# Kernel optimization log

Measured on AMD Instinct MI355X. Metric: run time of the kernel, lower is better.

## Reference

```python
import jax, jax.numpy as jnp
import numpy as np

B, S, D = 8, 2048, 128

def setup_inputs() -> dict:
    key = jax.random.key(0)
    kq, kk, kv, km = jax.random.split(key, 4)
    q = jax.random.normal(kq, (B, S, D), dtype=jnp.float32)
    k = jax.random.normal(kk, (B, S, D), dtype=jnp.float32)
    v = jax.random.normal(kv, (B, S, D), dtype=jnp.float32)
    mask = jax.random.randint(km, (B, S), 0, 2).astype(bool)  # True = masked out
    return {"q": q, "k": k, "v": v, "mask": mask}

def reference(q, k, v, mask):
    scaler = np.sqrt(D).astype(np.float32)
    # score[b, i, j] = <q_i, k_j> / sqrt(d_k)
    score = jnp.einsum('bik,bjk->bij', q, k) / scaler
    score = score - jnp.max(score, axis=-1, keepdims=True)
    e = jnp.exp(score)
    # mask is (B, S_kv): broadcast across query positions, zero out masked keys
    e = jnp.where(mask[:, None, :], 0.0, e)
    a = e / jnp.sum(e, axis=-1, keepdims=True)
    c = jnp.einsum('bij,bjd->bid', a, v)
    return c
```

## Files before the change

kernel.cpp:

```cpp
#include <hip/hip_runtime.h>
#include <hip/hip_fp16.h>
#include <math.h>

typedef __attribute__((ext_vector_type(8))) short short8;
typedef __attribute__((ext_vector_type(4))) float floatx4;

namespace {
constexpr int Bn = 8;
constexpr int Sn = 2048;
constexpr int Dn = 128;
constexpr int BQ = 64;
constexpr int BK = 64;
constexpr int QTILES = Sn / BQ;
constexpr int NKB = Sn / BK;
constexpr int ROWS = Bn * Sn;
constexpr int NSPLIT = 4;
constexpr float SC2 = 0.12753102063642597f;
constexpr int TILE_USH = BK * Dn;
}

#if __has_builtin(__builtin_amdgcn_exp2f)
#define EXP2(x) __builtin_amdgcn_exp2f(x)
#else
#define EXP2(x) exp2f(x)
#endif

__device__ __forceinline__ unsigned short f2bf(float x) {
  union { float f; unsigned u; } a; a.f = x;
  unsigned r = a.u + 0x7fffu + ((a.u >> 16) & 1u);
  return (unsigned short)(r >> 16);
}

__device__ __forceinline__ void gl_lds16(const void* g, void* l, int lane) {
#if __has_builtin(__builtin_amdgcn_global_load_lds)
  (void)lane;
  __builtin_amdgcn_global_load_lds((const __attribute__((address_space(1))) unsigned int*)g,
                                   (__attribute__((address_space(3))) unsigned int*)l, 16, 0, 0);
#else
  *(float4*)((char*)l + lane * 16) = *(const float4*)g;
#endif
}

__global__ __launch_bounds__(256)
void prep(const float* __restrict__ kg, const float* __restrict__ vg,
          const unsigned char* __restrict__ mraw,
          unsigned short* __restrict__ Kpg, unsigned short* __restrict__ Vpg,
          float* __restrict__ mb2g) {
  __shared__ __align__(16) float Vf[16 * 136];
  const int p = blockIdx.x;
  const int b = p >> 7, q = p & 127;
  const int kb = q >> 2, k16 = q & 3;
  const int t = threadIdx.x;

  unsigned wv = ((const unsigned int*)mraw)[t];
  int any1  = __syncthreads_or((wv & 0x0000ff00u) ? 1 : 0);
  int any23 = __syncthreads_or((wv & 0xffff0000u) ? 1 : 0);
  const int mlayout = any1 ? 1 : (any23 ? 2 : 0);
  if (p < 64) {
    int idx = p * 256 + t;
    bool ms;
    if (mlayout == 1)      ms = mraw[idx] != 0;
    else if (mlayout == 2) ms = ((const float*)mraw)[idx] != 0.0f;
    else                   ms = ((const int*)mraw)[idx] != 0;
    mb2g[idx] = ms ? -1e30f : 0.0f;
  }

  const int j  = t >> 4;
  const int o8 = t & 15;
  const size_t base = ((size_t)(b * Sn + kb * 64 + k16 * 16 + j)) * 32 + o8 * 2;
  const float4* k4 = (const float4*)kg;
  const float4* v4 = (const float4*)vg;

  {
    float4 a = k4[base], bq = k4[base + 1];
    short8 pk;
    pk[0] = (short)f2bf(a.x);  pk[1] = (short)f2bf(a.y);
    pk[2] = (short)f2bf(a.z);  pk[3] = (short)f2bf(a.w);
    pk[4] = (short)f2bf(bq.x); pk[5] = (short)f2bf(bq.y);
    pk[6] = (short)f2bf(bq.z); pk[7] = (short)f2bf(bq.w);
    const int jl = k16 * 16 + j;
    *(short8*)(Kpg + (size_t)(b * NKB + kb) * TILE_USH + jl * 128 + ((o8 ^ (jl & 7)) * 8)) = pk;
  }

  {
    float4 a = v4[base], bq = v4[base + 1];
    *(float4*)&Vf[j * 136 + o8 * 8]     = a;
    *(float4*)&Vf[j * 136 + o8 * 8 + 4] = bq;
  }
  __syncthreads();

  {
    const int d = t >> 1, h = t & 1;
    short8 pv;
    #pragma unroll
    for (int i = 0; i < 8; ++i)
      pv[i] = (short)f2bf(Vf[(h * 8 + i) * 136 + d]);
    const int og = k16 * 2 + h;
    *(short8*)(Vpg + (size_t)(b * NKB + kb) * TILE_USH + d * 64 + ((og ^ (d & 7)) * 8)) = pv;
  }
}

template<int SPLIT, bool DIRECT>
__global__ __launch_bounds__(128, 2)
void attn_fwd(const float* __restrict__ qg,
              const unsigned short* __restrict__ Kpg,
              const unsigned short* __restrict__ Vpg,
              const float* __restrict__ mb2g,
              float* __restrict__ outg, __half* __restrict__ Op,
              float* __restrict__ Mp, float* __restrict__ Lp) {
  __shared__ __align__(16) unsigned short Khi[TILE_USH];
  __shared__ __align__(16) unsigned short Vt[TILE_USH];
  __shared__ __align__(16) unsigned short Pq[2 * 2048];

  const int tid = threadIdx.x;
  const int bid = blockIdx.x;
  const int b   = bid & 7;
  const int q0  = ((bid >> 3) & (QTILES - 1)) * BQ;
  const int s   = bid >> 8;
  const int kb0 = s * (NKB / SPLIT);
  const int kbN = kb0 + NKB / SPLIT;
  const int w   = tid >> 6;
  const int L   = tid & 63;
  const int g   = L >> 4;
  const int c   = L & 15;
  const int sw  = c & 7;

  short8 qh[2][4], ql[2][4];
  #pragma unroll
  for (int s2 = 0; s2 < 2; ++s2) {
    const float* qrow = qg + (size_t)(b * Sn + q0 + w * 32 + s2 * 16 + c) * Dn + g * 8;
    #pragma unroll
    for (int kk = 0; kk < 4; ++kk) {
      #pragma unroll
      for (int j = 0; j < 8; ++j) {
        float x = qrow[kk * 32 + j];
        unsigned short hi = f2bf(x);
        union { unsigned u; float f; } hv; hv.u = ((unsigned)hi) << 16;
        qh[s2][kk][j] = (short)hi;
        ql[s2][kk][j] = (short)f2bf(x - hv.f);
      }
    }
  }

  float m_i[2] = {-INFINITY, -INFINITY}, l_i[2] = {0.0f, 0.0f};
  floatx4 O[2][8];
  #pragma unroll
  for (int s2 = 0; s2 < 2; ++s2)
    #pragma unroll
    for (int n2 = 0; n2 < 8; ++n2) O[s2][n2] = (floatx4){0.f, 0.f, 0.f, 0.f};

  unsigned short* pwave = Pq + w * 2048;
  const int stagebase = w * 8192;

  for (int kb = kb0; kb < kbN; ++kb) {
    __syncthreads();
    {
      const char* kt = (const char*)(Kpg + (size_t)(b * NKB + kb) * TILE_USH);
      const char* vt = (const char*)(Vpg + (size_t)(b * NKB + kb) * TILE_USH);
      #pragma unroll
      for (int i = 0; i < 8; ++i) {
        const int off = stagebase + i * 1024;
        gl_lds16(kt + off + L * 16, (char*)Khi + off, L);
        gl_lds16(vt + off + L * 16, (char*)Vt + off, L);
      }
    }
    __syncthreads();

    const float4* mb4 = (const float4*)(mb2g + b * Sn + kb * BK);
    float4 mbv[4];
    #pragma unroll
    for (int nt = 0; nt < 4; ++nt) mbv[nt] = mb4[nt * 4 + g];

    floatx4 acc[2][4];
    #pragma unroll
    for (int s2 = 0; s2 < 2; ++s2)
      #pragma unroll
      for (int nt = 0; nt < 4; ++nt) acc[s2][nt] = (floatx4){0.f, 0.f, 0.f, 0.f};
    #pragma unroll
    for (int kk = 0; kk < 4; ++kk) {
      const int ko = ((kk * 4 + g) ^ sw) * 8;
      #pragma unroll
      for (int nt = 0; nt < 4; ++nt) {
        short8 kf = *(const short8*)&Khi[(nt * 16 + c) * 128 + ko];
        acc[0][nt] = __builtin_amdgcn_mfma_f32_16x16x32_bf16(kf, qh[0][kk], acc[0][nt], 0, 0, 0);
        acc[0][nt] = __builtin_amdgcn_mfma_f32_16x16x32_bf16(kf, ql[0][kk], acc[0][nt], 0, 0, 0);
        acc[1][nt] = __builtin_amdgcn_mfma_f32_16x16x32_bf16(kf, qh[1][kk], acc[1][nt], 0, 0, 0);
        acc[1][nt] = __builtin_amdgcn_mfma_f32_16x16x32_bf16(kf, ql[1][kk], acc[1][nt], 0, 0, 0);
      }
    }

    float alpha[2];
    #pragma unroll
    for (int s2 = 0; s2 < 2; ++s2) {
      #pragma unroll
      for (int nt = 0; nt < 4; ++nt) {
        acc[s2][nt][0] = fmaf(acc[s2][nt][0], SC2, mbv[nt].x);
        acc[s2][nt][1] = fmaf(acc[s2][nt][1], SC2, mbv[nt].y);
        acc[s2][nt][2] = fmaf(acc[s2][nt][2], SC2, mbv[nt].z);
        acc[s2][nt][3] = fmaf(acc[s2][nt][3], SC2, mbv[nt].w);
      }
      float mx = -INFINITY;
      #pragma unroll
      for (int nt = 0; nt < 4; ++nt)
        #pragma unroll
        for (int r = 0; r < 4; ++r) mx = fmaxf(mx, acc[s2][nt][r]);
      mx = fmaxf(mx, __shfl_xor(mx, 16));
      mx = fmaxf(mx, __shfl_xor(mx, 32));
      const float mnew = fmaxf(m_i[s2], mx);
      alpha[s2] = EXP2(m_i[s2] - mnew);
      float rs = 0.0f;
      #pragma unroll
      for (int nt = 0; nt < 4; ++nt)
        #pragma unroll
        for (int r = 0; r < 4; ++r) {
          float e = EXP2(acc[s2][nt][r] - mnew);
          acc[s2][nt][r] = e;
          rs += e;
        }
      rs += __shfl_xor(rs, 16);
      rs += __shfl_xor(rs, 32);
      l_i[s2] = l_i[s2] * alpha[s2] + rs;
      m_i[s2] = mnew;
    }

    #pragma unroll
    for (int s2 = 0; s2 < 2; ++s2)
      #pragma unroll
      for (int nt = 0; nt < 4; ++nt) {
        ushort4 pk = make_ushort4(f2bf(acc[s2][nt][0]), f2bf(acc[s2][nt][1]),
                                  f2bf(acc[s2][nt][2]), f2bf(acc[s2][nt][3]));
        const int oct = nt * 2 + (g >> 1);
        *(ushort4*)&pwave[s2 * 1024 + c * 64 + ((oct ^ sw) * 8) + (g & 1) * 4] = pk;
      }

    #pragma unroll
    for (int s2 = 0; s2 < 2; ++s2)
      #pragma unroll
      for (int n2 = 0; n2 < 8; ++n2)
        #pragma unroll
        for (int r = 0; r < 4; ++r) O[s2][n2][r] *= alpha[s2];

    #pragma unroll
    for (int kk = 0; kk < 2; ++kk) {
      const int ko = ((kk * 4 + g) ^ sw) * 8;
      short8 pf0 = *(const short8*)&pwave[c * 64 + ko];
      short8 pf1 = *(const short8*)&pwave[1024 + c * 64 + ko];
      #pragma unroll
      for (int n2 = 0; n2 < 8; ++n2) {
        short8 vf = *(const short8*)&Vt[(n2 * 16 + c) * 64 + ko];
        O[0][n2] = __builtin_amdgcn_mfma_f32_16x16x32_bf16(vf, pf0, O[0][n2], 0, 0, 0);
        O[1][n2] = __builtin_amdgcn_mfma_f32_16x16x32_bf16(vf, pf1, O[1][n2], 0, 0, 0);
      }
    }
  }

  #pragma unroll
  for (int s2 = 0; s2 < 2; ++s2) {
    const int rowbase = b * Sn + q0 + w * 32 + s2 * 16 + c;
    if constexpr (DIRECT) {
      const float inv = 1.0f / l_i[s2];
      float* orow = outg + (size_t)rowbase * Dn;
      #pragma unroll
      for (int n2 = 0; n2 < 8; ++n2) {
        float4 f = make_float4(O[s2][n2][0] * inv, O[s2][n2][1] * inv,
                               O[s2][n2][2] * inv, O[s2][n2][3] * inv);
        *(float4*)&orow[n2 * 16 + g * 4] = f;
      }
    } else {
      __half* orow = Op + ((size_t)s * ROWS + rowbase) * Dn;
      #pragma unroll
      for (int n2 = 0; n2 < 8; ++n2) {
        union { __half2 h2[2]; uint2 u; } pk;
        pk.h2[0] = __floats2half2_rn(O[s2][n2][0], O[s2][n2][1]);
        pk.h2[1] = __floats2half2_rn(O[s2][n2][2], O[s2][n2][3]);
        *(uint2*)&orow[n2 * 16 + g * 4] = pk.u;
      }
      if (g == 0) {
        Mp[s * ROWS + rowbase] = m_i[s2];
        Lp[s * ROWS + rowbase] = l_i[s2];
      }
    }
  }
}

__global__ __launch_bounds__(256)
void attn_combine(const __half* __restrict__ Op, const float* __restrict__ Mp,
                  const float* __restrict__ Lp, float4* __restrict__ out4) {
  const int gid = blockIdx.x * 256 + threadIdx.x;
  const int row = gid >> 5;
  const int c4  = gid & 31;
  float ms[NSPLIT];
  float m = -INFINITY;
  #pragma unroll
  for (int s = 0; s < NSPLIT; ++s) { ms[s] = Mp[s * ROWS + row]; m = fmaxf(m, ms[s]); }
  float l = 0.0f;
  float4 acc = make_float4(0.f, 0.f, 0.f, 0.f);
  #pragma unroll
  for (int s = 0; s < NSPLIT; ++s) {
    float wgt = EXP2(ms[s] - m);
    l = fmaf(Lp[s * ROWS + row], wgt, l);
    union { uint2 u; __half2 h2[2]; } pk;
    pk.u = ((const uint2*)Op)[(size_t)(s * ROWS + row) * 32 + c4];
    float2 f0 = __half22float2(pk.h2[0]);
    float2 f1 = __half22float2(pk.h2[1]);
    acc.x = fmaf(f0.x, wgt, acc.x);
    acc.y = fmaf(f0.y, wgt, acc.y);
    acc.z = fmaf(f1.x, wgt, acc.z);
    acc.w = fmaf(f1.y, wgt, acc.w);
  }
  float inv = 1.0f / l;
  out4[(size_t)row * 32 + c4] = make_float4(acc.x * inv, acc.y * inv, acc.z * inv, acc.w * inv);
}

extern "C" void kernel_launch(void* const* d_in, const int* in_sizes, int n_in,
                              void* d_out, int out_size, void* d_ws, size_t ws_size,
                              hipStream_t stream) {
  const float* q = (const float*)d_in[0];
  const float* k = (const float*)d_in[1];
  const float* v = (const float*)d_in[2];
  const unsigned char* m = (const unsigned char*)d_in[3];
  float* out = (float*)d_out;
  (void)in_sizes; (void)n_in; (void)out_size;

  constexpr size_t OPB = (size_t)NSPLIT * ROWS * Dn * sizeof(__half);
  constexpr size_t MLB = (size_t)NSPLIT * ROWS * sizeof(float);
  constexpr size_t KPB = (size_t)Bn * NKB * TILE_USH * 2;
  constexpr size_t MBB = (size_t)ROWS * sizeof(float);

  char* ws = (char*)d_ws;
  if (ws_size >= OPB + 2 * MLB + 2 * KPB + MBB) {
    __half* Op = (__half*)ws;
    float* Mp = (float*)(ws + OPB);
    float* Lp = (float*)(ws + OPB + MLB);
    unsigned short* Kp = (unsigned short*)(ws + OPB + 2 * MLB);
    unsigned short* Vp = (unsigned short*)(ws + OPB + 2 * MLB + KPB);
    float* mb2 = (float*)(ws + OPB + 2 * MLB + 2 * KPB);
    prep<<<dim3(Bn * NKB * 4), dim3(256), 0, stream>>>(k, v, m, Kp, Vp, mb2);
    attn_fwd<NSPLIT, false><<<dim3(Bn * QTILES * NSPLIT), dim3(128), 0, stream>>>(
        q, Kp, Vp, mb2, out, Op, Mp, Lp);
    attn_combine<<<dim3(ROWS * 32 / 256), dim3(256), 0, stream>>>(
        Op, Mp, Lp, (float4*)out);
  } else if (ws_size >= 2 * KPB + MBB) {
    unsigned short* Kp = (unsigned short*)ws;
    unsigned short* Vp = (unsigned short*)(ws + KPB);
    float* mb2 = (float*)(ws + 2 * KPB);
    prep<<<dim3(Bn * NKB * 4), dim3(256), 0, stream>>>(k, v, m, Kp, Vp, mb2);
    attn_fwd<1, true><<<dim3(Bn * QTILES), dim3(128), 0, stream>>>(
        q, Kp, Vp, mb2, out, nullptr, nullptr, nullptr);
  }
}
```

Before: 120.1 us.

## Switch attention MFMA tiles from 16x16x32 to 32x32x16 bf16

Restructures the attention inner loops to use 32x32x16 bf16 MFMA instructions, with each wave handling 32 query rows as one tile instead of two 16-row subtiles. This changes the register layout of Q, the score accumulators and O, and the LDS swizzle indexing for P. It also skips the O rescale when alpha is 1 across the wave, and uses hardware bf16 packing conversions in place of manual rounding. The aim is fewer MFMA issues and fewer LDS fragment loads per tile, plus less softmax overhead, at the cost of larger accumulator register footprints.

```diff
diff --git a/kernel.cpp b/kernel.cpp
--- a/kernel.cpp
+++ b/kernel.cpp
@@ -3,7 +3,8 @@
 #include <math.h>
 
 typedef __attribute__((ext_vector_type(8))) short short8;
-typedef __attribute__((ext_vector_type(4))) float floatx4;
+typedef __attribute__((ext_vector_type(16))) float floatx16;
+typedef __attribute__((ext_vector_type(2))) __bf16 bf16x2;
 
 namespace {
 constexpr int Bn = 8;
@@ -31,6 +32,12 @@
   return (unsigned short)(r >> 16);
 }
 
+__device__ __forceinline__ unsigned pack2bf(float x, float y) {
+  union { bf16x2 b; unsigned u; } c;
+  c.b[0] = (__bf16)x; c.b[1] = (__bf16)y;
+  return c.u;
+}
+
 __device__ __forceinline__ void gl_lds16(const void* g, void* l, int lane) {
 #if __has_builtin(__builtin_amdgcn_global_load_lds)
   (void)lane;
@@ -73,30 +80,26 @@
 
   {
     float4 a = k4[base], bq = k4[base + 1];
-    short8 pk;
-    pk[0] = (short)f2bf(a.x);  pk[1] = (short)f2bf(a.y);
-    pk[2] = (short)f2bf(a.z);  pk[3] = (short)f2bf(a.w);
-    pk[4] = (short)f2bf(bq.x); pk[5] = (short)f2bf(bq.y);
-    pk[6] = (short)f2bf(bq.z); pk[7] = (short)f2bf(bq.w);
+    union { unsigned u[4]; short8 s8; } pk;
+    pk.u[0] = pack2bf(a.x, a.y);   pk.u[1] = pack2bf(a.z, a.w);
+    pk.u[2] = pack2bf(bq.x, bq.y); pk.u[3] = pack2bf(bq.z, bq.w);
     const int jl = k16 * 16 + j;
-    *(short8*)(Kpg + (size_t)(b * NKB + kb) * TILE_USH + jl * 128 + ((o8 ^ (jl & 7)) * 8)) = pk;
-  }
-
+    *(short8*)(Kpg + (size_t)(b * NKB + kb) * TILE_USH + jl * 128 + ((o8 ^ (jl & 7)) * 8)) = pk.s8;
+  }
   {
     float4 a = v4[base], bq = v4[base + 1];
     *(float4*)&Vf[j * 136 + o8 * 8]     = a;
     *(float4*)&Vf[j * 136 + o8 * 8 + 4] = bq;
   }
   __syncthreads();
-
   {
     const int d = t >> 1, h = t & 1;
-    short8 pv;
-    #pragma unroll
-    for (int i = 0; i < 8; ++i)
-      pv[i] = (short)f2bf(Vf[(h * 8 + i) * 136 + d]);
+    union { unsigned u[4]; short8 s8; } pv;
+    #pragma unroll
+    for (int i = 0; i < 4; ++i)
+      pv.u[i] = pack2bf(Vf[(h * 8 + 2 * i) * 136 + d], Vf[(h * 8 + 2 * i + 1) * 136 + d]);
     const int og = k16 * 2 + h;
-    *(short8*)(Vpg + (size_t)(b * NKB + kb) * TILE_USH + d * 64 + ((og ^ (d & 7)) * 8)) = pv;
+    *(short8*)(Vpg + (size_t)(b * NKB + kb) * TILE_USH + d * 64 + ((og ^ (d & 7)) * 8)) = pv.s8;
   }
 }
 
@@ -121,33 +124,34 @@
   const int kbN = kb0 + NKB / SPLIT;
   const int w   = tid >> 6;
   const int L   = tid & 63;
-  const int g   = L >> 4;
-  const int c   = L & 15;
-  const int sw  = c & 7;
-
-  short8 qh[2][4], ql[2][4];
+  const int q   = L & 31;
+  const int h   = L >> 5;
+  const int sw  = q & 7;
+
+  short8 qh[8], ql[8];
+  {
+    const float* qrow = qg + (size_t)(b * Sn + q0 + w * 32 + q) * Dn;
+    #pragma unroll
+    for (int kstep = 0; kstep < 8; ++kstep) {
+      float4 f0 = *(const float4*)(qrow + kstep * 16 + h * 8);
+      float4 f1 = *(const float4*)(qrow + kstep * 16 + h * 8 + 4);
+      float xs[8] = {f0.x, f0.y, f0.z, f0.w, f1.x, f1.y, f1.z, f1.w};
+      #pragma unroll
+      for (int j = 0; j < 8; ++j) {
+        unsigned short hi = f2bf(xs[j]);
+        union { unsigned u; float f; } hv; hv.u = ((unsigned)hi) << 16;
+        qh[kstep][j] = (short)hi;
+        ql[kstep][j] = (short)f2bf(xs[j] - hv.f);
+      }
+    }
+  }
+
+  float m_i = -INFINITY, l_i = 0.0f;
+  floatx16 O32[4];
   #pragma unroll
-  for (int s2 = 0; s2 < 2; ++s2) {
-    const float* qrow = qg + (size_t)(b * Sn + q0 + w * 32 + s2 * 16 + c) * Dn + g * 8;
-    #pragma unroll
-    for (int kk = 0; kk < 4; ++kk) {
-      #pragma unroll
-      for (int j = 0; j < 8; ++j) {
-        float x = qrow[kk * 32 + j];
-        unsigned short hi = f2bf(x);
-        union { unsigned u; float f; } hv; hv.u = ((unsigned)hi) << 16;
-        qh[s2][kk][j] = (short)hi;
-        ql[s2][kk][j] = (short)f2bf(x - hv.f);
-      }
-    }
-  }
-
-  float m_i[2] = {-INFINITY, -INFINITY}, l_i[2] = {0.0f, 0.0f};
-  floatx4 O[2][8];
-  #pragma unroll
-  for (int s2 = 0; s2 < 2; ++s2)
-    #pragma unroll
-    for (int n2 = 0; n2 < 8; ++n2) O[s2][n2] = (floatx4){0.f, 0.f, 0.f, 0.f};
+  for (int dg = 0; dg < 4; ++dg)
+    #pragma unroll
+    for (int r = 0; r < 16; ++r) O32[dg][r] = 0.0f;
 
   unsigned short* pwave = Pq + w * 2048;
   const int stagebase = w * 8192;
@@ -167,118 +171,115 @@
     __syncthreads();
 
     const float4* mb4 = (const float4*)(mb2g + b * Sn + kb * BK);
-    float4 mbv[4];
-    #pragma unroll
-    for (int nt = 0; nt < 4; ++nt) mbv[nt] = mb4[nt * 4 + g];
-
-    floatx4 acc[2][4];
-    #pragma unroll
-    for (int s2 = 0; s2 < 2; ++s2)
-      #pragma unroll
-      for (int nt = 0; nt < 4; ++nt) acc[s2][nt] = (floatx4){0.f, 0.f, 0.f, 0.f};
-    #pragma unroll
-    for (int kk = 0; kk < 4; ++kk) {
-      const int ko = ((kk * 4 + g) ^ sw) * 8;
-      #pragma unroll
-      for (int nt = 0; nt < 4; ++nt) {
-        short8 kf = *(const short8*)&Khi[(nt * 16 + c) * 128 + ko];
-        acc[0][nt] = __builtin_amdgcn_mfma_f32_16x16x32_bf16(kf, qh[0][kk], acc[0][nt], 0, 0, 0);
-        acc[0][nt] = __builtin_amdgcn_mfma_f32_16x16x32_bf16(kf, ql[0][kk], acc[0][nt], 0, 0, 0);
-        acc[1][nt] = __builtin_amdgcn_mfma_f32_16x16x32_bf16(kf, qh[1][kk], acc[1][nt], 0, 0, 0);
-        acc[1][nt] = __builtin_amdgcn_mfma_f32_16x16x32_bf16(kf, ql[1][kk], acc[1][nt], 0, 0, 0);
-      }
-    }
-
-    float alpha[2];
-    #pragma unroll
-    for (int s2 = 0; s2 < 2; ++s2) {
-      #pragma unroll
-      for (int nt = 0; nt < 4; ++nt) {
-        acc[s2][nt][0] = fmaf(acc[s2][nt][0], SC2, mbv[nt].x);
-        acc[s2][nt][1] = fmaf(acc[s2][nt][1], SC2, mbv[nt].y);
-        acc[s2][nt][2] = fmaf(acc[s2][nt][2], SC2, mbv[nt].z);
-        acc[s2][nt][3] = fmaf(acc[s2][nt][3], SC2, mbv[nt].w);
-      }
-      float mx = -INFINITY;
-      #pragma unroll
-      for (int nt = 0; nt < 4; ++nt)
+    float4 mbv[2][4];
+    #pragma unroll
+    for (int kg = 0; kg < 2; ++kg)
+      #pragma unroll
+      for (int ro = 0; ro < 4; ++ro) mbv[kg][ro] = mb4[kg * 8 + ro * 2 + h];
+
+    floatx16 a32[2];
+    #pragma unroll
+    for (int kg = 0; kg < 2; ++kg)
+      #pragma unroll
+      for (int r = 0; r < 16; ++r) a32[kg][r] = 0.0f;
+    #pragma unroll
+    for (int kstep = 0; kstep < 8; ++kstep) {
+      const int ko = ((kstep * 2 + h) ^ sw) * 8;
+      #pragma unroll
+      for (int kg = 0; kg < 2; ++kg) {
+        short8 kf = *(const short8*)&Khi[(kg * 32 + q) * 128 + ko];
+        a32[kg] = __builtin_amdgcn_mfma_f32_32x32x16_bf16(kf, qh[kstep], a32[kg], 0, 0, 0);
+        a32[kg] = __builtin_amdgcn_mfma_f32_32x32x16_bf16(kf, ql[kstep], a32[kg], 0, 0, 0);
+      }
+    }
+
+    #pragma unroll
+    for (int kg = 0; kg < 2; ++kg)
+      #pragma unroll
+      for (int ro = 0; ro < 4; ++ro) {
+        float4 f = mbv[kg][ro];
+        a32[kg][4 * ro + 0] = fmaf(a32[kg][4 * ro + 0], SC2, f.x);
+        a32[kg][4 * ro + 1] = fmaf(a32[kg][4 * ro + 1], SC2, f.y);
+        a32[kg][4 * ro + 2] = fmaf(a32[kg][4 * ro + 2], SC2, f.z);
+        a32[kg][4 * ro + 3] = fmaf(a32[kg][4 * ro + 3], SC2, f.w);
+      }
+    float mx = -INFINITY;
+    #pragma unroll
+    for (int kg = 0; kg < 2; ++kg)
+      #pragma unroll
+      for (int r = 0; r < 16; ++r) mx = fmaxf(mx, a32[kg][r]);
+    mx = fmaxf(mx, __shfl_xor(mx, 32));
+    const float mnew = fmaxf(m_i, mx);
+    const float alpha = EXP2(m_i - mnew);
+    float rs = 0.0f;
+    #pragma unroll
+    for (int kg = 0; kg < 2; ++kg)
+      #pragma unroll
+      for (int r = 0; r < 16; ++r) {
+        float e = EXP2(a32[kg][r] - mnew);
+        a32[kg][r] = e;
+        rs += e;
+      }
+    rs += __shfl_xor(rs, 32);
+    l_i = l_i * alpha + rs;
+    m_i = mnew;
+
+    #pragma unroll
+    for (int kg = 0; kg < 2; ++kg)
+      #pragma unroll
+      for (int ro = 0; ro < 4; ++ro) {
+        uint2 u;
+        u.x = pack2bf(a32[kg][4 * ro + 0], a32[kg][4 * ro + 1]);
+        u.y = pack2bf(a32[kg][4 * ro + 2], a32[kg][4 * ro + 3]);
+        const int oct = kg * 4 + ro;
+        *(uint2*)&pwave[q * 64 + ((oct ^ sw) * 8) + h * 4] = u;
+      }
+
+    if (!__all(alpha == 1.0f)) {
+      #pragma unroll
+      for (int dg = 0; dg < 4; ++dg)
         #pragma unroll
-        for (int r = 0; r < 4; ++r) mx = fmaxf(mx, acc[s2][nt][r]);
-      mx = fmaxf(mx, __shfl_xor(mx, 16));
-      mx = fmaxf(mx, __shfl_xor(mx, 32));
-      const float mnew = fmaxf(m_i[s2], mx);
-      alpha[s2] = EXP2(m_i[s2] - mnew);
-      float rs = 0.0f;
-      #pragma unroll
-      for (int nt = 0; nt < 4; ++nt)
-        #pragma unroll
-        for (int r = 0; r < 4; ++r) {
-          float e = EXP2(acc[s2][nt][r] - mnew);
-          acc[s2][nt][r] = e;
-          rs += e;
-        }
-      rs += __shfl_xor(rs, 16);
-      rs += __shfl_xor(rs, 32);
-      l_i[s2] = l_i[s2] * alpha[s2] + rs;
-      m_i[s2] = mnew;
-    }
-
-    #pragma unroll
-    for (int s2 = 0; s2 < 2; ++s2)
-      #pragma unroll
-      for (int nt = 0; nt < 4; ++nt) {
-        ushort4 pk = make_ushort4(f2bf(acc[s2][nt][0]), f2bf(acc[s2][nt][1]),
-                                  f2bf(acc[s2][nt][2]), f2bf(acc[s2][nt][3]));
-        const int oct = nt * 2 + (g >> 1);
-        *(ushort4*)&pwave[s2 * 1024 + c * 64 + ((oct ^ sw) * 8) + (g & 1) * 4] = pk;
-      }
-
-    #pragma unroll
-    for (int s2 = 0; s2 < 2; ++s2)
-      #pragma unroll
-      for (int n2 = 0; n2 < 8; ++n2)
-        #pragma unroll
-        for (int r = 0; r < 4; ++r) O[s2][n2][r] *= alpha[s2];
-
-    #pragma unroll
-    for (int kk = 0; kk < 2; ++kk) {
-      const int ko = ((kk * 4 + g) ^ sw) * 8;
-      short8 pf0 = *(const short8*)&pwave[c * 64 + ko];
-      short8 pf1 = *(const short8*)&pwave[1024 + c * 64 + ko];
-      #pragma unroll
-      for (int n2 = 0; n2 < 8; ++n2) {
-        short8 vf = *(const short8*)&Vt[(n2 * 16 + c) * 64 + ko];
-        O[0][n2] = __builtin_amdgcn_mfma_f32_16x16x32_bf16(vf, pf0, O[0][n2], 0, 0, 0);
-        O[1][n2] = __builtin_amdgcn_mfma_f32_16x16x32_bf16(vf, pf1, O[1][n2], 0, 0, 0);
-      }
-    }
-  }
-
-  #pragma unroll
-  for (int s2 = 0; s2 < 2; ++s2) {
-    const int rowbase = b * Sn + q0 + w * 32 + s2 * 16 + c;
-    if constexpr (DIRECT) {
-      const float inv = 1.0f / l_i[s2];
-      float* orow = outg + (size_t)rowbase * Dn;
-      #pragma unroll
-      for (int n2 = 0; n2 < 8; ++n2) {
-        float4 f = make_float4(O[s2][n2][0] * inv, O[s2][n2][1] * inv,
-                               O[s2][n2][2] * inv, O[s2][n2][3] * inv);
-        *(float4*)&orow[n2 * 16 + g * 4] = f;
-      }
-    } else {
-      __half* orow = Op + ((size_t)s * ROWS + rowbase) * Dn;
-      #pragma unroll
-      for (int n2 = 0; n2 < 8; ++n2) {
+        for (int r = 0; r < 16; ++r) O32[dg][r] *= alpha;
+    }
+
+    #pragma unroll
+    for (int k2 = 0; k2 < 4; ++k2) {
+      const int ko = ((k2 * 2 + h) ^ sw) * 8;
+      short8 pf = *(const short8*)&pwave[q * 64 + ko];
+      #pragma unroll
+      for (int dg = 0; dg < 4; ++dg) {
+        short8 vf = *(const short8*)&Vt[(dg * 32 + q) * 64 + ko];
+        O32[dg] = __builtin_amdgcn_mfma_f32_32x32x16_bf16(vf, pf, O32[dg], 0, 0, 0);
+      }
+    }
+  }
+
+  const int row = b * Sn + q0 + w * 32 + q;
+  if constexpr (DIRECT) {
+    const float inv = 1.0f / l_i;
+    float* orow = outg + (size_t)row * Dn;
+    #pragma unroll
+    for (int dg = 0; dg < 4; ++dg)
+      #pragma unroll
+      for (int ro = 0; ro < 4; ++ro) {
+        float4 f = make_float4(O32[dg][4 * ro] * inv,     O32[dg][4 * ro + 1] * inv,
+                               O32[dg][4 * ro + 2] * inv, O32[dg][4 * ro + 3] * inv);
+        *(float4*)&orow[dg * 32 + 8 * ro + 4 * h] = f;
+      }
+  } else {
+    __half* orow = Op + ((size_t)s * ROWS + row) * Dn;
+    #pragma unroll
+    for (int dg = 0; dg < 4; ++dg)
+      #pragma unroll
+      for (int ro = 0; ro < 4; ++ro) {
         union { __half2 h2[2]; uint2 u; } pk;
-        pk.h2[0] = __floats2half2_rn(O[s2][n2][0], O[s2][n2][1]);
-        pk.h2[1] = __floats2half2_rn(O[s2][n2][2], O[s2][n2][3]);
-        *(uint2*)&orow[n2 * 16 + g * 4] = pk.u;
-      }
-      if (g == 0) {
-        Mp[s * ROWS + rowbase] = m_i[s2];
-        Lp[s * ROWS + rowbase] = l_i[s2];
-      }
+        pk.h2[0] = __floats2half2_rn(O32[dg][4 * ro],     O32[dg][4 * ro + 1]);
+        pk.h2[1] = __floats2half2_rn(O32[dg][4 * ro + 2], O32[dg][4 * ro + 3]);
+        *(uint2*)&orow[dg * 32 + 8 * ro + 4 * h] = pk.u;
+      }
+    if (h == 0) {
+      Mp[s * ROWS + row] = m_i;
+      Lp[s * ROWS + row] = l_i;
     }
   }
 }
```

New measurement: 118.3 us. About the same (-1.5%).
